# Performance work log

Measured on AMD Instinct MI355X. Metric: run time of the kernel, lower is better.

## Reference

```python
import jax, jax.numpy as jnp
import numpy as np

SCALE = 64 ** -0.5
MAX_LR = 0.01


def newtonschulz5(t, steps=5, eps=1e-7, coefs=(3.4445, -4.775, 2.0315)):
    # t: [h, i, j]; orthogonalize via quintic Newton-Schulz iteration
    a, b, c = coefs
    should_transpose = t.shape[-2] > t.shape[-1]
    if should_transpose:
        t = jnp.swapaxes(t, -1, -2)
    norm = jnp.sqrt(jnp.sum(t * t, axis=(-1, -2), keepdims=True))
    t = t / jnp.maximum(norm, eps)
    for _ in range(steps):
        A = t @ jnp.swapaxes(t, -1, -2)
        B = b * A + c * (A @ A)
        t = a * t + B @ t
    if should_transpose:
        t = jnp.swapaxes(t, -1, -2)
    return t


def setup_inputs() -> dict:
    key = jax.random.key(0)
    ks = jax.random.split(key, 7)
    b, n, d, h, dh = 2, 2048, 512, 8, 64
    s = 0.05  # scale random weights for numerical sanity (softmax not one-hot)
    return {
        "tokens": jax.random.normal(ks[0], (b, n, d), jnp.float32),
        "rms_weight": jnp.ones((d,), jnp.float32),
        "wq": jax.random.normal(ks[1], (h, d, dh), jnp.float32) * s,
        "wk": jax.random.normal(ks[2], (h, d, dh), jnp.float32) * s,
        "wv": jax.random.normal(ks[3], (h, d, dh), jnp.float32) * s,
        "wo": jax.random.normal(ks[4], (h, dh, d), jnp.float32) * s,
        "lr_w": jax.random.normal(ks[5], (1, d), jnp.float32) * s,
        "tv_w": jax.random.normal(ks[6], (d, d), jnp.float32) * s,
        "return_next_memories": 1,
    }


def reference(tokens, rms_weight, wq, wk, wv, wo, lr_w, tv_w, return_next_memories):
    eps = jnp.finfo(tokens.dtype).eps
    # RMSNorm (torch nn.RMSNorm with eps=None -> finfo eps)
    t = tokens * jax.lax.rsqrt(jnp.mean(tokens * tokens, axis=-1, keepdims=True) + eps) * rms_weight

    q = jnp.einsum('bnd,hde->bhne', t, wq)  # [b,h,n,dh]
    k = jnp.einsum('bnd,hde->bhne', t, wk)
    v = jnp.einsum('bnd,hde->bhne', t, wv)

    score = jnp.einsum('bhie,bhje->bhij', q, k) * SCALE
    n = score.shape[-1]
    causal_mask = jnp.triu(jnp.ones((n, n), bool), 1)
    score = jnp.where(causal_mask, -jnp.finfo(score.dtype).max, score)
    attn = jax.nn.softmax(score, axis=-1)
    out = jnp.einsum('bhij,bhje->bhie', attn, v)  # [b,h,n,dh]
    pred_values = jnp.einsum('bhne,hed->bnd', out, wo)

    if not return_next_memories:
        return pred_values

    # target values: Linear(dim,dim,no bias) + LayerNorm(no affine) on shifted tokens
    tv = jnp.einsum('bnd,od->bno', t[:, 1:], tv_w)
    mu = jnp.mean(tv, axis=-1, keepdims=True)
    var = jnp.var(tv, axis=-1, keepdims=True)
    target_values = (tv - mu) * jax.lax.rsqrt(var + 1e-5)

    tok = t[:, :-1]                       # [b,n-1,d]
    pred_fw = pred_values[:, :-1]
    out_t = out[:, :, :-1]
    attn_t = attn[:, :, :-1, :-1]
    q_t, k_t, v_t = q[:, :, :-1], k[:, :, :-1], v[:, :, :-1]

    lr = jax.nn.sigmoid(jnp.einsum('bnd,od->bno', tok, lr_w)) * MAX_LR  # [b,n-1,1]
    error = (target_values - pred_fw) * lr

    dout = jnp.einsum('bnd,hed->bhne', error, wo)            # [b,h,n-1,dh]
    dwo = jnp.einsum('bnd,bhne->hed', error, out_t)          # [h,dh,d]
    delta = jnp.sum(dout * out_t, axis=-1, keepdims=True)    # [b,h,n-1,1]
    dv = jnp.einsum('bhij,bhie->bhje', attn_t, dout)
    dattn = jnp.einsum('bhje,bhie->bhij', v_t, dout)
    dscore = SCALE * attn_t * (dattn - delta)
    dq = jnp.einsum('bhje,bhij->bhie', k_t, dscore)
    dk = jnp.einsum('bhie,bhij->bhje', q_t, dscore)
    dwq = jnp.einsum('bhie,bid->hde', dq, tok)
    dwk = jnp.einsum('bhje,bjd->hde', dk, tok)
    dwv = jnp.einsum('bhje,bjd->hde', dv, tok)

    # muon update: Newton-Schulz orthogonalization of value/output fast-weight grads
    dwv = newtonschulz5(dwv)
    dwo = newtonschulz5(dwo)

    return (pred_values, dwq, dwk, dwv, dwo)
```

## Files before the change

kernel.cpp:

```cpp
#include <hip/hip_runtime.h>
#include <float.h>
#include <math.h>

#define B_   2
#define N_   2048
#define D_   512
#define H_   8
#define DH_  64
#define NM_  2047
#define SCALE_F 0.125f
#define LBK 72

typedef __attribute__((ext_vector_type(8))) short bf16x8;
typedef __attribute__((ext_vector_type(4))) float f32x4;
#define MFMA_B16(a,b,c) __builtin_amdgcn_mfma_f32_16x16x32_bf16(a,b,c,0,0,0)

__device__ __forceinline__ short f2bf(float f){
  unsigned u = __float_as_uint(f);
  unsigned r = u + 0x7fffu + ((u>>16)&1u);
  return (short)(r>>16);
}
__device__ __forceinline__ float bf2f(short s){
  return __uint_as_float(((unsigned)(unsigned short)s)<<16);
}
// ... 121 lines not shown
    outt[(size_t)(c0+rr)*4096 + r0+cc]=l[rr][cc];
  }
}
__global__ __launch_bounds__(256) void k_trans_f(const float* __restrict__ in,
    short* __restrict__ outn, short* __restrict__ outt){
  __shared__ short l[64][66];
  int r0=blockIdx.x<<6, c0=blockIdx.y<<6, tid=threadIdx.x;
  for(int kk=0;kk<16;kk++){
    int idx=kk*256+tid, rr=idx>>6, cc=idx&63;
    short v=f2bf(in[(size_t)(r0+rr)*512 + c0+cc]);
    outn[(size_t)(r0+rr)*512 + c0+cc]=v;
    l[cc][rr]=v;
  }
  __syncthreads();
  for(int kk=0;kk<16;kk++){
    int idx=kk*256+tid, rr=idx>>6, cc=idx&63;
    outt[(size_t)(c0+rr)*4096 + r0+cc]=l[rr][cc];
  }
}

__global__ __launch_bounds__(256) void k_gemm_qkv(const short* __restrict__ tb,
    const short* __restrict__ wqt, const short* __restrict__ wkt, const short* __restrict__ wvt,
    short* __restrict__ qh, short* __restrict__ kh, short* __restrict__ vh,
    short* __restrict__ qt, short* __restrict__ kt, short* __restrict__ vt){
  __shared__ __attribute__((aligned(16))) short as[64][LBK], bs[64][LBK];
  int r0=blockIdx.x<<6, ct=blockIdx.y, which=ct>>3, h=ct&7;
  const short* Bt=(which==0?wqt:which==1?wkt:wvt)+(size_t)h*32768;
  f32x4 acc[4];
  #pragma unroll
  for(int nb=0;nb<4;nb++) acc[nb]=(f32x4){0.f,0.f,0.f,0.f};
  gemm64(tb+(size_t)r0*512, 512, Bt, 512, 8, as, bs, acc);
  short* on=(which==0?qh:which==1?kh:vh);
  short* ot=(which==0?qt:which==1?kt:vt);
  int tid=threadIdx.x, w=tid>>6, lane=tid&63, lg=lane>>4, ln=lane&15;
  size_t bh=(size_t)(r0>>11)*8+h;
  int n0=(r0&2047)+w*16+lg*4;
  #pragma unroll
  for(int nb=0;nb<4;nb++){
    int e=nb*16+ln;
    short4 s4;
    s4.x=f2bf(acc[nb][0]); s4.y=f2bf(acc[nb][1]);
    s4.z=f2bf(acc[nb][2]); s4.w=f2bf(acc[nb][3]);
    on[(bh*2048+n0  )*64+e]=s4.x;
    on[(bh*2048+n0+1)*64+e]=s4.y;
    on[(bh*2048+n0+2)*64+e]=s4.z;
    on[(bh*2048+n0+3)*64+e]=s4.w;
    *(short4*)&ot[(bh*64+e)*2048+n0]=s4;
  }
}

__global__ __launch_bounds__(256) void k_fa_fwd(const short* __restrict__ qh,
    const short* __restrict__ kh, const short* __restrict__ vt,
    float* __restrict__ op0, float* __restrict__ op1, float* __restrict__ mlb){
  int bh = blockIdx.x, qq = blockIdx.y, half = blockIdx.z;
  int it = (qq<16)? (31-qq) : (qq-16);
  int i0 = it<<6;
  const short* qhb = qh + (size_t)bh*N_*DH_;
  const short* khb = kh + (size_t)bh*N_*DH_;
  const short* vtb = vt + (size_t)bh*DH_*N_;
  __shared__ __attribute__((aligned(16))) short ks[64][LBK], vts[64][LBK];
  __shared__ __attribute__((aligned(16))) short psb[4][16][LBK];
  int tid=threadIdx.x, w=tid>>6, lane=tid&63, lg=lane>>4, ln=lane&15;
  bf16x8 aq[2];
  #pragma unroll
  for(int s=0;s<2;s++)
    aq[s] = *(const bf16x8*)&qhb[(size_t)(i0+w*16+ln)*DH_ + 32*s + lg*8];
  f32x4 acc[4];
  float mrow[4], lrow[4];
  #pragma unroll
  for(int nb=0;nb<4;nb++) acc[nb]=(f32x4){0.f,0.f,0.f,0.f};
  #pragma unroll
  for(int r=0;r<4;r++){ mrow[r]=-FLT_MAX; lrow[r]=0.f; }
  int4 ka0,ka1,va0,va1;
  tload(khb+(size_t)half*64*DH_, DH_, tid, ka0,ka1);
  tload(vtb+half*64, N_, tid, va0,va1);
  for(int jt=half;jt<=it;jt+=2){
    int j0 = jt<<6;
    bool diag = (jt==it);
    __syncthreads();
    twrite(ks, tid, ka0,ka1);
    twrite(vts, tid, va0,va1);
    if(jt+2<=it){
      tload(khb+(size_t)(jt+2)*64*DH_, DH_, tid, ka0,ka1);
      tload(vtb+(jt+2)*64, N_, tid, va0,va1);
    }
    __syncthreads();
    f32x4 sv[4];
    __builtin_amdgcn_s_setprio(1);
    #pragma unroll
    for(int nb=0;nb<4;nb++){
      f32x4 z = {0.f,0.f,0.f,0.f};
      #pragma unroll
      for(int s=0;s<2;s++){
        bf16x8 bk = *(const bf16x8*)&ks[nb*16+ln][32*s + lg*8];
        z = MFMA_B16(aq[s], bk, z);
      }
      sv[nb]=z;
    }
    __builtin_amdgcn_s_setprio(0);
    int iiB = i0 + w*16 + lg*4;
    #pragma unroll
    for(int r=0;r<4;r++){
      int ii = iiB + r;
      float srow[4]; float mx = -FLT_MAX;
      if(diag){
        #pragma unroll
        for(int nb=0;nb<4;nb++){
          float x = sv[nb][r]*SCALE_F;
          if(j0+nb*16+ln > ii) x = -FLT_MAX;
          srow[nb]=x; mx=fmaxf(mx,x);
        }
      } else {
        #pragma unroll
        for(int nb=0;nb<4;nb++){
          float x = sv[nb][r]*SCALE_F;
          srow[nb]=x; mx=fmaxf(mx,x);
        }
      }
      mx=fmaxf(mx,__shfl_xor(mx,1)); mx=fmaxf(mx,__shfl_xor(mx,2));
      mx=fmaxf(mx,__shfl_xor(mx,4)); mx=fmaxf(mx,__shfl_xor(mx,8));
      float mn = fmaxf(mrow[r], mx);
      float rs = 0.f;
      #pragma unroll
      for(int nb=0;nb<4;nb++){
        float pv = __expf(srow[nb]-mn);
        psb[w][lg*4+r][ln+16*nb]=f2bf(pv); rs+=pv;
      }
      rs+=__shfl_xor(rs,1); rs+=__shfl_xor(rs,2);
      rs+=__shfl_xor(rs,4); rs+=__shfl_xor(rs,8);
      float corr = __expf(mrow[r]-mn);
      lrow[r]=lrow[r]*corr+rs; mrow[r]=mn;
      #pragma unroll
      for(int nb=0;nb<4;nb++) acc[nb][r]*=corr;
    }
    lds_fence();
    __builtin_amdgcn_s_setprio(1);
    #pragma unroll
    for(int nb=0;nb<4;nb++){
      #pragma unroll
      for(int s=0;s<2;s++){
        bf16x8 pa = *(const bf16x8*)&psb[w][ln][32*s + lg*8];
        bf16x8 bv = *(const bf16x8*)&vts[nb*16+ln][32*s + lg*8];
        acc[nb] = MFMA_B16(pa, bv, acc[nb]);
      }
    }
    __builtin_amdgcn_s_setprio(0);
    lds_fence();
  }
  float* op   = half? op1 : op0;
  float* marr = mlb + half*65536;
  float* larr = marr + 32768;
  #pragma unroll
  for(int r=0;r<4;r++){
    int ii = i0 + w*16 + lg*4 + r;
    size_t row = (size_t)bh*2048 + ii;
    #pragma unroll
    for(int nb=0;nb<4;nb++)
      op[row*64 + nb*16+ln] = acc[nb][r];
    if(ln==0){ marr[row]=mrow[r]; larr[row]=lrow[r]; }
  }
}

__global__ __launch_bounds__(256) void k_fa_merge(const float* __restrict__ op0,
    const float* __restrict__ op1, const float* __restrict__ mlb,
    short* __restrict__ obb, float* __restrict__ lse){
  int row = blockIdx.x*4 + (threadIdx.x>>6);
  int lane = threadIdx.x&63;
  float m0 = mlb[row],        l0 = mlb[32768+row];
  float m1 = mlb[65536+row],  l1 = mlb[98304+row];
  float m  = fmaxf(m0,m1);
  float c0 = __expf(m0-m), c1 = __expf(m1-m);
  float l  = l0*c0 + l1*c1;
  float o  = (op0[(size_t)row*64+lane]*c0 + op1[(size_t)row*64+lane]*c1)/l;
  int bh = row>>11, i = row&2047, b = bh>>3, h = bh&7;
  obb[((size_t)(b*2048+i))*512 + h*64 + lane] = f2bf(o);
  if(lane==0) lse[row] = m + logf(l);
}

__global__ __launch_bounds__(256) void k_gemm_pred(const short* __restrict__ obb,
    const short* __restrict__ wot, float* __restrict__ pred){
  __shared__ __attribute__((aligned(16))) short as[64][LBK], bs[64][LBK];
  int r0=blockIdx.x<<6, c0=blockIdx.y<<6;
  f32x4 acc[4];
  #pragma unroll
  for(int nb=0;nb<4;nb++) acc[nb]=(f32x4){0.f,0.f,0.f,0.f};
  gemm64(obb+(size_t)r0*512, 512, wot+(size_t)c0*512, 512, 8, as, bs, acc);
  int tid=threadIdx.x, w=tid>>6, lane=tid&63, lg=lane>>4, ln=lane&15;
  int row=r0+w*16+lg*4;
  #pragma unroll
  for(int nb=0;nb<4;nb++)
    #pragma unroll
    for(int r=0;r<4;r++)
      pred[(size_t)(row+r)*512 + c0+nb*16+ln]=acc[nb][r];
}

__global__ __launch_bounds__(256) void k_gemm_tv(const short* __restrict__ tb,
    const short* __restrict__ tvwb, float* __restrict__ er){
  __shared__ __attribute__((aligned(16))) short as[64][LBK], bs[64][LBK];
  int r0=blockIdx.x<<6, c0=blockIdx.y<<6;
  f32x4 acc[4];
  #pragma unroll
  for(int nb=0;nb<4;nb++) acc[nb]=(f32x4){0.f,0.f,0.f,0.f};
  gemm64(tb+(size_t)(r0+1)*512, 512, tvwb+(size_t)c0*512, 512, 8, as, bs, acc);
  int tid=threadIdx.x, w=tid>>6, lane=tid&63, lg=lane>>4, ln=lane&15;
  int row=r0+w*16+lg*4;
  #pragma unroll
  for(int nb=0;nb<4;nb++)
    #pragma unroll
    for(int r=0;r<4;r++){
      float v=(((row+r)&2047)==2047)?0.f:acc[nb][r];
      er[(size_t)(row+r)*512 + c0+nb*16+ln]=v;
    }
// ... 20 lines not shown
  float S2=r2[0]+r2[1]+r2[2]+r2[3];
  float S3=r3[0]+r3[1]+r3[2]+r3[3];
  float mu  = S1*(1.f/512.f);
  float var = S2*(1.f/512.f) - mu*mu;
  float rstd= rsqrtf(var + 1e-5f);
  float lr  = 0.01f/(1.f+__expf(-S3));
  tv[tid]     = ((v0-mu)*rstd - pr[tid])*lr;
  tv[tid+256] = ((v1-mu)*rstd - pr[tid+256])*lr;
}

__global__ __launch_bounds__(256) void k_gemm_dout(const short* __restrict__ erb,
    const short* __restrict__ wob, short* __restrict__ doh, short* __restrict__ dot){
  __shared__ __attribute__((aligned(16))) short as[64][LBK], bs[64][LBK];
  int r0=blockIdx.x<<6, h=blockIdx.y;
  f32x4 acc[4];
  #pragma unroll
  for(int nb=0;nb<4;nb++) acc[nb]=(f32x4){0.f,0.f,0.f,0.f};
  gemm64(erb+(size_t)r0*512, 512, wob+(size_t)h*32768, 512, 8, as, bs, acc);
  int tid=threadIdx.x, w=tid>>6, lane=tid&63, lg=lane>>4, ln=lane&15;
  size_t bh=(size_t)(r0>>11)*8+h;
  int n0=(r0&2047)+w*16+lg*4;
  #pragma unroll
  for(int nb=0;nb<4;nb++){
    int e=nb*16+ln;
    short4 s4;
    s4.x=f2bf(acc[nb][0]); s4.y=f2bf(acc[nb][1]);
    s4.z=f2bf(acc[nb][2]); s4.w=f2bf(acc[nb][3]);
    doh[(bh*2048+n0  )*64+e]=s4.x;
    doh[(bh*2048+n0+1)*64+e]=s4.y;
    doh[(bh*2048+n0+2)*64+e]=s4.z;
    doh[(bh*2048+n0+3)*64+e]=s4.w;
    *(short4*)&dot[(bh*64+e)*2048+n0]=s4;
  }
}

__global__ __launch_bounds__(256) void k_delta(const short* __restrict__ doh,
    const short* __restrict__ obb, float* __restrict__ delta){
  int rid = blockIdx.x*4 + (threadIdx.x>>6);
  int lane = threadIdx.x&63;
  if(rid >= B_*H_*NM_) return;
  int b = rid/(H_*NM_); int rem = rid - b*H_*NM_;
  int h = rem/NM_; int i = rem - h*NM_;
  float v = bf2f(doh[((size_t)(b*H_+h)*N_ + i)*DH_ + lane])
          * bf2f(obb[((size_t)(b*N_+i))*D_ + h*DH_ + lane]);
  v = wred64(v);
  if(lane==0) delta[((size_t)(b*H_+h))*N_ + i] = v;
}

__global__ __launch_bounds__(256) void k_fa_dq(const short* __restrict__ qh,
    const short* __restrict__ kh, const short* __restrict__ vh,
    const short* __restrict__ kt, const short* __restrict__ doh,
    const float* __restrict__ lse, const float* __restrict__ delta,
    short* __restrict__ dqt, short* __restrict__ dqp1){
  int bh = blockIdx.x, it = blockIdx.y, half = blockIdx.z;
  int i0 = it<<6;
  const short* qhb = qh + (size_t)bh*N_*DH_;
  const short* khb = kh + (size_t)bh*N_*DH_;
  const short* vhb = vh + (size_t)bh*N_*DH_;
  const short* ktb = kt + (size_t)bh*DH_*N_;
  const short* dohb= doh+ (size_t)bh*N_*DH_;
  __shared__ __attribute__((aligned(16))) short ks[64][LBK], vs[64][LBK], kts[64][LBK];
  __shared__ __attribute__((aligned(16))) short psb[4][16][LBK];
  int tid=threadIdx.x, w=tid>>6, lane=tid&63, lg=lane>>4, ln=lane&15;
  bf16x8 aq[2], ad[2];
  float Lr[4], dl[4];
  #pragma unroll
  for(int s=0;s<2;s++){
    aq[s]=*(const bf16x8*)&qhb[(size_t)(i0+w*16+ln)*DH_+32*s+lg*8];
    ad[s]=*(const bf16x8*)&dohb[(size_t)(i0+w*16+ln)*DH_+32*s+lg*8];
  }
  #pragma unroll
  for(int r=0;r<4;r++){
    int ii=i0+w*16+lg*4+r;
    Lr[r]=lse[(size_t)bh*N_+ii];
    dl[r]=(ii<NM_)?delta[(size_t)bh*N_+ii]:0.f;
  }
  f32x4 acc[4];
  #pragma unroll
  for(int nb=0;nb<4;nb++) acc[nb]=(f32x4){0.f,0.f,0.f,0.f};
  int4 ka0,ka1,va0,va1,ta0,ta1;
  tload(khb+(size_t)half*64*DH_, DH_, tid, ka0,ka1);
  tload(vhb+(size_t)half*64*DH_, DH_, tid, va0,va1);
  tload(ktb+half*64, N_, tid, ta0,ta1);
  for(int jt=half;jt<=it;jt+=2){
    int j0=jt<<6;
    bool msk_needed = (jt==it) || (it==31);
    __syncthreads();
    twrite(ks, tid, ka0,ka1);
    twrite(vs, tid, va0,va1);
    twrite(kts, tid, ta0,ta1);
    if(jt+2<=it){
      tload(khb+(size_t)(jt+2)*64*DH_, DH_, tid, ka0,ka1);
      tload(vhb+(size_t)(jt+2)*64*DH_, DH_, tid, va0,va1);
      tload(ktb+(jt+2)*64, N_, tid, ta0,ta1);
    }
    __syncthreads();
    f32x4 sv[4], dav[4];
    __builtin_amdgcn_s_setprio(1);
    #pragma unroll
    for(int nb=0;nb<4;nb++){
      f32x4 z={0.f,0.f,0.f,0.f}, zd={0.f,0.f,0.f,0.f};
      #pragma unroll
      for(int s=0;s<2;s++){
        bf16x8 bk=*(const bf16x8*)&ks[nb*16+ln][32*s+lg*8];
        bf16x8 bv=*(const bf16x8*)&vs[nb*16+ln][32*s+lg*8];
        z = MFMA_B16(aq[s], bk, z);
        zd= MFMA_B16(ad[s], bv, zd);
      }
      sv[nb]=z; dav[nb]=zd;
    }
    __builtin_amdgcn_s_setprio(0);
    if(msk_needed){
      #pragma unroll
      for(int r=0;r<4;r++){
        int ii=i0+w*16+lg*4+r;
        #pragma unroll
        for(int nb=0;nb<4;nb++){
          int jj=j0+nb*16+ln;
          float pv=__expf(sv[nb][r]*SCALE_F - Lr[r]);
          float dsv=SCALE_F*pv*(dav[nb][r]-dl[r]);
          if(jj>ii || ii>=NM_ || jj>=NM_) dsv=0.f;
          psb[w][lg*4+r][ln+16*nb]=f2bf(dsv);
        }
      }
    } else {
      #pragma unroll
      for(int r=0;r<4;r++)
        #pragma unroll
        for(int nb=0;nb<4;nb++){
          float pv=__expf(sv[nb][r]*SCALE_F - Lr[r]);
          psb[w][lg*4+r][ln+16*nb]=f2bf(SCALE_F*pv*(dav[nb][r]-dl[r]));
        }
    }
    lds_fence();
    __builtin_amdgcn_s_setprio(1);
    #pragma unroll
    for(int nb=0;nb<4;nb++){
      #pragma unroll
      for(int s=0;s<2;s++){
        bf16x8 pa = *(const bf16x8*)&psb[w][ln][32*s+lg*8];
        bf16x8 bk = *(const bf16x8*)&kts[nb*16+ln][32*s+lg*8];
        acc[nb]=MFMA_B16(pa,bk,acc[nb]);
      }
    }
    __builtin_amdgcn_s_setprio(0);
    lds_fence();
  }
  short* dst = half? dqp1 : dqt;
  #pragma unroll
  for(int nb=0;nb<4;nb++){
    short4 s4;
    s4.x=f2bf(acc[nb][0]); s4.y=f2bf(acc[nb][1]);
    s4.z=f2bf(acc[nb][2]); s4.w=f2bf(acc[nb][3]);
    *(short4*)&dst[((size_t)bh*64 + nb*16+ln)*2048 + i0+w*16+lg*4]=s4;
  }
}

__global__ __launch_bounds__(256) void k_dqred(short* __restrict__ dqt,
    const short* __restrict__ dqp1){
  size_t i = ((size_t)blockIdx.x*256 + threadIdx.x)*8;
  int4 a = *(const int4*)&dqt[i];
  int4 b = *(const int4*)&dqp1[i];
  short* pa=(short*)&a; const short* pb=(const short*)&b;
  short out[8];
  #pragma unroll
  for(int k=0;k<8;k++) out[k]=f2bf(bf2f(pa[k])+bf2f(pb[k]));
  *(int4*)&dqt[i] = *(int4*)out;
}

__global__ __launch_bounds__(256) void k_fa_dkv(const short* __restrict__ kh,
    const short* __restrict__ vh, const short* __restrict__ qh,
    const short* __restrict__ qt, const short* __restrict__ doh,
    const short* __restrict__ dot,
    const float* __restrict__ lse, const float* __restrict__ delta,
    short* __restrict__ dkt, short* __restrict__ dvt,
    short* __restrict__ dkp1, short* __restrict__ dvp1){
  int bh = blockIdx.x, jt = blockIdx.y, half = blockIdx.z;
  int j0 = jt<<6;
  const short* khb = kh + (size_t)bh*N_*DH_;
  const short* vhb = vh + (size_t)bh*N_*DH_;
  const short* qhb = qh + (size_t)bh*N_*DH_;
  const short* qtb = qt + (size_t)bh*DH_*N_;
  const short* dohb= doh+ (size_t)bh*N_*DH_;
  const short* dotb= dot+ (size_t)bh*DH_*N_;
  __shared__ __attribute__((aligned(16))) short qs[64][LBK], dos[64][LBK], qts[64][LBK], dots[64][LBK];
  __shared__ __attribute__((aligned(16))) short psv[4][16][LBK], psk[4][16][LBK];
  __shared__ float Ls[64], dls[64];
  int tid=threadIdx.x, w=tid>>6, lane=tid&63, lg=lane>>4, ln=lane&15;
  bf16x8 akf[2], avf[2];
  #pragma unroll
  for(int s=0;s<2;s++){
    akf[s]=*(const bf16x8*)&khb[(size_t)(j0+w*16+ln)*DH_+32*s+lg*8];
    avf[s]=*(const bf16x8*)&vhb[(size_t)(j0+w*16+ln)*DH_+32*s+lg*8];
  }
  f32x4 accv[4], acck[4];
  #pragma unroll
  for(int nb=0;nb<4;nb++){
    accv[nb]=(f32x4){0.f,0.f,0.f,0.f};
    acck[nb]=(f32x4){0.f,0.f,0.f,0.f};
  }
  int it0 = jt + half;
  int4 qa0,qa1,da0,da1,qta0,qta1,dta0,dta1;
  float Lnx=0.f, dlnx=0.f;
  {
    int ip = (it0<32)? (it0<<6) : 0;
    tload(qhb+(size_t)ip*DH_, DH_, tid, qa0,qa1);
    tload(dohb+(size_t)ip*DH_, DH_, tid, da0,da1);
    tload(qtb+ip, N_, tid, qta0,qta1);
    tload(dotb+ip, N_, tid, dta0,dta1);
    if(tid<64){
      int ii=ip+tid;
      Lnx=lse[(size_t)bh*N_+ii];
      dlnx=(ii<NM_)?delta[(size_t)bh*N_+ii]:0.f;
    }
  }
  for(int it=it0; it<32; it+=2){
    int i0=it<<6;
    bool msk_needed = (it==jt) || (it==31);
    __syncthreads();
    twrite(qs, tid, qa0,qa1);
    twrite(dos, tid, da0,da1);
    twrite(qts, tid, qta0,qta1);
    twrite(dots, tid, dta0,dta1);
    if(tid<64){ Ls[tid]=Lnx; dls[tid]=dlnx; }
    if(it+2<32){
      int i1=(it+2)<<6;
      tload(qhb+(size_t)i1*DH_, DH_, tid, qa0,qa1);
      tload(dohb+(size_t)i1*DH_, DH_, tid, da0,da1);
      tload(qtb+i1, N_, tid, qta0,qta1);
      tload(dotb+i1, N_, tid, dta0,dta1);
      if(tid<64){
        int ii=i1+tid;
        Lnx=lse[(size_t)bh*N_+ii];
        dlnx=(ii<NM_)?delta[(size_t)bh*N_+ii]:0.f;
      }
    }
    __syncthreads();
    f32x4 sv[4], dav[4];
    __builtin_amdgcn_s_setprio(1);
    #pragma unroll
    for(int nb=0;nb<4;nb++){
      f32x4 z={0.f,0.f,0.f,0.f}, zd={0.f,0.f,0.f,0.f};
      #pragma unroll
      for(int s=0;s<2;s++){
        bf16x8 bq=*(const bf16x8*)&qs[nb*16+ln][32*s+lg*8];
        bf16x8 bd=*(const bf16x8*)&dos[nb*16+ln][32*s+lg*8];
        z = MFMA_B16(akf[s], bq, z);
        zd= MFMA_B16(avf[s], bd, zd);
      }
      sv[nb]=z; dav[nb]=zd;
    }
    __builtin_amdgcn_s_setprio(0);
    if(msk_needed){
      #pragma unroll
      for(int nb=0;nb<4;nb++){
        float Lc=Ls[nb*16+ln], dlc=dls[nb*16+ln];
        int ii=i0+nb*16+ln;
        #pragma unroll
        for(int r=0;r<4;r++){
          int jj=j0+w*16+lg*4+r;
          float pv=__expf(sv[nb][r]*SCALE_F - Lc);
          bool msk=(jj>ii)||(ii>=NM_)||(jj>=NM_);
          if(msk) pv=0.f;
          float ds = msk?0.f: SCALE_F*pv*(dav[nb][r]-dlc);
          psv[w][lg*4+r][ln+16*nb]=f2bf(pv);
          psk[w][lg*4+r][ln+16*nb]=f2bf(ds);
        }
      }
    } else {
      #pragma unroll
      for(int nb=0;nb<4;nb++){
        float Lc=Ls[nb*16+ln], dlc=dls[nb*16+ln];
        #pragma unroll
        for(int r=0;r<4;r++){
          float pv=__expf(sv[nb][r]*SCALE_F - Lc);
          psv[w][lg*4+r][ln+16*nb]=f2bf(pv);
          psk[w][lg*4+r][ln+16*nb]=f2bf(SCALE_F*pv*(dav[nb][r]-dlc));
        }
      }
    }
    lds_fence();
    __builtin_amdgcn_s_setprio(1);
    #pragma unroll
    for(int nb=0;nb<4;nb++){
      #pragma unroll
      for(int s=0;s<2;s++){
        bf16x8 pa = *(const bf16x8*)&psv[w][ln][32*s+lg*8];
        bf16x8 bd = *(const bf16x8*)&dots[nb*16+ln][32*s+lg*8];
        accv[nb]=MFMA_B16(pa,bd,accv[nb]);
        bf16x8 pk = *(const bf16x8*)&psk[w][ln][32*s+lg*8];
        bf16x8 bq = *(const bf16x8*)&qts[nb*16+ln][32*s+lg*8];
        acck[nb]=MFMA_B16(pk,bq,acck[nb]);
      }
    }
    __builtin_amdgcn_s_setprio(0);
    lds_fence();
  }
  short* dvd = half? dvp1 : dvt;
  short* dkd = half? dkp1 : dkt;
  #pragma unroll
  for(int nb=0;nb<4;nb++){
    int e=nb*16+ln, n0=j0+w*16+lg*4;
    short4 s4;
    s4.x=f2bf(accv[nb][0]); s4.y=f2bf(accv[nb][1]);
    s4.z=f2bf(accv[nb][2]); s4.w=f2bf(accv[nb][3]);
    *(short4*)&dvd[((size_t)bh*64+e)*2048 + n0]=s4;
    s4.x=f2bf(acck[nb][0]); s4.y=f2bf(acck[nb][1]);
    s4.z=f2bf(acck[nb][2]); s4.w=f2bf(acck[nb][3]);
    *(short4*)&dkd[((size_t)bh*64+e)*2048 + n0]=s4;
  }
}

__global__ __launch_bounds__(256) void k_dkvred(short* __restrict__ dkt,
    short* __restrict__ dvt, const short* __restrict__ dkp1,
    const short* __restrict__ dvp1){
  int bid = blockIdx.x;
  short* dst; const short* src;
  if(bid<1024){ dst=dkt; src=dkp1; } else { dst=dvt; src=dvp1; bid-=1024; }
  size_t i = ((size_t)bid*256 + threadIdx.x)*8;
  int4 a = *(const int4*)&dst[i];
  int4 b = *(const int4*)&src[i];
  short* pa=(short*)&a; const short* pb=(const short*)&b;
  short out[8];
  #pragma unroll
  for(int k=0;k<8;k++) out[k]=f2bf(bf2f(pa[k])+bf2f(pb[k]));
  *(int4*)&dst[i] = *(int4*)out;
}

__global__ __launch_bounds__(256) void k_gemm_wgq(const short* __restrict__ tt,
    const short* __restrict__ g, float* __restrict__ par){
  __shared__ __attribute__((aligned(16))) short as[64][LBK], bs[64][LBK];
  int dt=blockIdx.x, h=blockIdx.y, sp=blockIdx.z;
  int b=sp>>2, n0b=(sp&3)*512;
  f32x4 acc[4];
  #pragma unroll
  for(int nb=0;nb<4;nb++) acc[nb]=(f32x4){0.f,0.f,0.f,0.f};
  gemm64(tt + (size_t)(dt*64)*4096 + sp*512, 4096,
         g  + ((size_t)(b*8+h)*64)*2048 + n0b, 2048, 8, as, bs, acc);
  int tid=threadIdx.x, w=tid>>6, lane=tid&63, lg=lane>>4, ln=lane&15;
  int row=w*16+lg*4;
  #pragma unroll
  for(int nb=0;nb<4;nb++)
    #pragma unroll
    for(int r=0;r<4;r++)
      par[(size_t)sp*262144 + (size_t)h*32768 + (size_t)(dt*64+row+r)*64 + nb*16+ln]=acc[nb][r];
}

__global__ __launch_bounds__(256) void k_gemm_wgo(const short* __restrict__ outt,
    const short* __restrict__ ert, float* __restrict__ par){
  __shared__ __attribute__((aligned(16))) short as[64][LBK], bs[64][LBK];
  int ct=blockIdx.x, h=blockIdx.y, sp=blockIdx.z;
  f32x4 acc[4];
  #pragma unroll
  for(int nb=0;nb<4;nb++) acc[nb]=(f32x4){0.f,0.f,0.f,0.f};
  gemm64(outt + (size_t)(h*64)*4096 + sp*512, 4096,
         ert  + (size_t)(ct*64)*4096 + sp*512, 4096, 8, as, bs, acc);
  int tid=threadIdx.x, w=tid>>6, lane=tid&63, lg=lane>>4, ln=lane&15;
  int row=w*16+lg*4;
  #pragma unroll
  for(int nb=0;nb<4;nb++)
    #pragma unroll
    for(int r=0;r<4;r++)
// ... 125 lines not shown
  const float* wq   =(const float*)d_in[2];
  const float* wk   =(const float*)d_in[3];
  const float* wv   =(const float*)d_in[4];
  const float* wo   =(const float*)d_in[5];
  const float* lrw  =(const float*)d_in[6];
  const float* tvw  =(const float*)d_in[7];
  float* out = (float*)d_out;
  float* ws  = (float*)d_ws;

  short* tb   = (short*)(ws);
  short* tt   = (short*)(ws + 1064960);
  short* qh   = (short*)(ws + 2113536);
  short* kh   = (short*)(ws + 3162112);
  short* vh   = (short*)(ws + 4210688);
  short* qt   = (short*)(ws + 5259264);
  short* kt   = (short*)(ws + 6307840);
  short* vt   = (short*)(ws + 7356416);
  float* er_  = ws + 8404992;
  float* op0  = ws + 8404992;
  short* dqp1 = (short*)(ws + 8404992);
  short* dkp1 = (short*)(ws + 8404992);
  short* dvp1 = (short*)(ws + 9453568);
  short* obb  = (short*)(ws + 10502144);
  short* outt = (short*)(ws + 11550720);
  short* erb  = (short*)(ws + 12599296);
  short* ert  = (short*)(ws + 13647872);
  short* doh  = (short*)(ws + 14696448);
  short* dot  = (short*)(ws + 15745024);
  float* par_ = ws + 14696448;
  float* op1  = ws + 14696448;
  short* dqt  = (short*)(ws + 16793600);
  float* mlb  = ws + 16793600;
  short* dkt  = (short*)(ws + 17842176);
  short* dvt  = (short*)(ws + 18890752);
  short* wqt  = (short*)(ws + 19939328);
  short* wkt  = (short*)(ws + 20070400);
  short* wvt  = (short*)(ws + 20201472);
  short* wob  = (short*)(ws + 20332544);
  short* wot  = (short*)(ws + 20463616);
  short* tvwb = (short*)(ws + 20594688);
  float* lse_ = ws + 20725760;
  float* dlt_ = ws + 20758528;
  float* X0_  = ws + 20791296;

  float* OUT_PRED = out;
  float* OUT_DWQ  = out + 2097152;
  float* OUT_DWK  = out + 2359296;
  float* OUT_DWV  = out + 2621440;
  float* OUT_DWO  = out + 2883584;

  k_rmsnorm<<<4160,256,0,stream>>>(tokens, rmsw, tb);
  k_wprep<<<272,256,0,stream>>>(wq,wk,wv,wo,tvw, wqt,wkt,wvt,wob,wot,tvwb);
  k_gemm_qkv<<<dim3(64,24),256,0,stream>>>(tb, wqt,wkt,wvt, qh,kh,vh, qt,kt,vt);
  k_fa_fwd<<<dim3(16,32,2),256,0,stream>>>(qh, kh, vt, op0, op1, mlb);
  k_fa_merge<<<8192,256,0,stream>>>(op0, op1, mlb, obb, lse_);
  k_gemm_pred<<<dim3(64,8),256,0,stream>>>(obb, wot, OUT_PRED);

  if(out_size < 3145728) return;

  k_trans_b<<<dim3(64,8),256,0,stream>>>(tb, tt);
  k_gemm_tv<<<dim3(64,8),256,0,stream>>>(tb, tvwb, er_);
  k_lnerr<<<4094,256,0,stream>>>(er_, tb, OUT_PRED, lrw);
  k_trans_f<<<dim3(64,8),256,0,stream>>>(er_, erb, ert);
  k_gemm_dout<<<dim3(64,8),256,0,stream>>>(erb, wob, doh, dot);
  k_delta<<<8188,256,0,stream>>>(doh, obb, dlt_);
  k_fa_dq<<<dim3(16,32,2),256,0,stream>>>(qh, kh, vh, kt, doh, lse_, dlt_, dqt, dqp1);
  k_dqred<<<1024,256,0,stream>>>(dqt, dqp1);
  k_fa_dkv<<<dim3(16,32,2),256,0,stream>>>(kh, vh, qh, qt, doh, dot, lse_, dlt_,
                                           dkt, dvt, dkp1, dvp1);
  k_dkvred<<<2048,256,0,stream>>>(dkt, dvt, dkp1, dvp1);
  k_trans_b<<<dim3(64,8),256,0,stream>>>(obb, outt);

  k_gemm_wgq<<<dim3(8,8,8),256,0,stream>>>(tt, dqt, par_);
  k_wred_direct<<<1024,256,0,stream>>>(par_, OUT_DWQ);
  k_gemm_wgq<<<dim3(8,8,8),256,0,stream>>>(tt, dkt, par_);
  k_wred_direct<<<1024,256,0,stream>>>(par_, OUT_DWK);
  k_gemm_wgq<<<dim3(8,8,8),256,0,stream>>>(tt, dvt, par_);
  k_wred_xv<<<1024,256,0,stream>>>(par_, X0_);
  k_gemm_wgo<<<dim3(8,8,8),256,0,stream>>>(outt, ert, par_);
  k_wred_xo<<<1024,256,0,stream>>>(par_, X0_);

  k_ns_fused<<<16,1024,0,stream>>>(X0_, OUT_DWV, OUT_DWO);
}
```

Baseline: 311.1 us.

## Process two adjacent 64-row tiles per block in flash-attention kernels

The forward, dQ and dKV attention kernels now have each block handle a pair of adjacent query (or key) tiles. Every K/V (or Q/dO) tile staged into LDS is reused for both tiles, and the grid is halved from 1024 to 512 blocks. Blocks are paired so work stays balanced across the causal triangle. This cuts global-to-LDS traffic and barrier count per unit of work, at the cost of roughly double the registers and LDS per block and fewer blocks to spread across the CUs.

```diff
diff --git a/kernel.cpp b/kernel.cpp
--- a/kernel.cpp
+++ b/kernel.cpp
@@ -197,86 +197,102 @@
 __global__ __launch_bounds__(256) void k_fa_fwd(const short* __restrict__ qh,
     const short* __restrict__ kh, const short* __restrict__ vt,
     float* __restrict__ op0, float* __restrict__ op1, float* __restrict__ mlb){
-  int bh = blockIdx.x, qq = blockIdx.y, half = blockIdx.z;
-  int it = (qq<16)? (31-qq) : (qq-16);
-  int i0 = it<<6;
+  int bh = blockIdx.x, y = blockIdx.y;
+  int a    = (y<16)? y : 31-y;
+  int half = (y<16)? 0 : 1;
+  int itA = 2*a, itB = 2*a+1;
   const short* qhb = qh + (size_t)bh*N_*DH_;
   const short* khb = kh + (size_t)bh*N_*DH_;
   const short* vtb = vt + (size_t)bh*DH_*N_;
   __shared__ __attribute__((aligned(16))) short ks[64][LBK], vts[64][LBK];
-  __shared__ __attribute__((aligned(16))) short psb[4][16][LBK];
+  __shared__ __attribute__((aligned(16))) short psb[2][4][16][LBK];
   int tid=threadIdx.x, w=tid>>6, lane=tid&63, lg=lane>>4, ln=lane&15;
-  bf16x8 aq[2];
-  #pragma unroll
-  for(int s=0;s<2;s++)
-    aq[s] = *(const bf16x8*)&qhb[(size_t)(i0+w*16+ln)*DH_ + 32*s + lg*8];
-  f32x4 acc[4];
-  float mrow[4], lrow[4];
-  #pragma unroll
-  for(int nb=0;nb<4;nb++) acc[nb]=(f32x4){0.f,0.f,0.f,0.f};
-  #pragma unroll
-  for(int r=0;r<4;r++){ mrow[r]=-FLT_MAX; lrow[r]=0.f; }
+  bf16x8 aq[2][2];
+  #pragma unroll
+  for(int sd=0;sd<2;sd++){
+    int i0=(sd?itB:itA)<<6;
+    #pragma unroll
+    for(int s=0;s<2;s++)
+      aq[sd][s] = *(const bf16x8*)&qhb[(size_t)(i0+w*16+ln)*DH_ + 32*s + lg*8];
+  }
+  f32x4 acc[2][4];
+  float mrow[2][4], lrow[2][4];
+  #pragma unroll
+  for(int sd=0;sd<2;sd++){
+    #pragma unroll
+    for(int nb=0;nb<4;nb++) acc[sd][nb]=(f32x4){0.f,0.f,0.f,0.f};
+    #pragma unroll
+    for(int r=0;r<4;r++){ mrow[sd][r]=-FLT_MAX; lrow[sd][r]=0.f; }
+  }
   int4 ka0,ka1,va0,va1;
   tload(khb+(size_t)half*64*DH_, DH_, tid, ka0,ka1);
   tload(vtb+half*64, N_, tid, va0,va1);
-  for(int jt=half;jt<=it;jt+=2){
+  for(int jt=half;jt<=itB;jt+=2){
     int j0 = jt<<6;
-    bool diag = (jt==it);
+    bool actA = (jt<=itA);
     __syncthreads();
     twrite(ks, tid, ka0,ka1);
     twrite(vts, tid, va0,va1);
-    if(jt+2<=it){
+    if(jt+2<=itB){
       tload(khb+(size_t)(jt+2)*64*DH_, DH_, tid, ka0,ka1);
       tload(vtb+(jt+2)*64, N_, tid, va0,va1);
     }
     __syncthreads();
-    f32x4 sv[4];
+    f32x4 sv[2][4];
     __builtin_amdgcn_s_setprio(1);
     #pragma unroll
     for(int nb=0;nb<4;nb++){
-      f32x4 z = {0.f,0.f,0.f,0.f};
+      f32x4 z0={0.f,0.f,0.f,0.f}, z1={0.f,0.f,0.f,0.f};
       #pragma unroll
       for(int s=0;s<2;s++){
         bf16x8 bk = *(const bf16x8*)&ks[nb*16+ln][32*s + lg*8];
-        z = MFMA_B16(aq[s], bk, z);
-      }
-      sv[nb]=z;
+        z0 = MFMA_B16(aq[0][s], bk, z0);
+        z1 = MFMA_B16(aq[1][s], bk, z1);
+      }
+      sv[0][nb]=z0; sv[1][nb]=z1;
     }
     __builtin_amdgcn_s_setprio(0);
-    int iiB = i0 + w*16 + lg*4;
-    #pragma unroll
-    for(int r=0;r<4;r++){
-      int ii = iiB + r;
-      float srow[4]; float mx = -FLT_MAX;
-      if(diag){
+    #pragma unroll
+    for(int sd=0;sd<2;sd++){
+      if(sd==0 && !actA) continue;
+      int it_ = sd? itB : itA;
+      int i0  = it_<<6;
+      bool diag = (jt==it_);
+      int iiB = i0 + w*16 + lg*4;
+      #pragma unroll
+      for(int r=0;r<4;r++){
+        int ii = iiB + r;
+        float srow[4]; float mx = -FLT_MAX;
+        if(diag){
+          #pragma unroll
+          for(int nb=0;nb<4;nb++){
+            float x = sv[sd][nb][r]*SCALE_F;
+            if(j0+nb*16+ln > ii) x = -FLT_MAX;
+            srow[nb]=x; mx=fmaxf(mx,x);
+          }
+        } else {
+          #pragma unroll
+          for(int nb=0;nb<4;nb++){
+            float x = sv[sd][nb][r]*SCALE_F;
+            srow[nb]=x; mx=fmaxf(mx,x);
+          }
+        }
+        mx=fmaxf(mx,__shfl_xor(mx,1)); mx=fmaxf(mx,__shfl_xor(mx,2));
+        mx=fmaxf(mx,__shfl_xor(mx,4)); mx=fmaxf(mx,__shfl_xor(mx,8));
+        float mn = fmaxf(mrow[sd][r], mx);
+        float rs = 0.f;
         #pragma unroll
         for(int nb=0;nb<4;nb++){
-          float x = sv[nb][r]*SCALE_F;
-          if(j0+nb*16+ln > ii) x = -FLT_MAX;
-          srow[nb]=x; mx=fmaxf(mx,x);
+          float pv = __expf(srow[nb]-mn);
+          psb[sd][w][lg*4+r][ln+16*nb]=f2bf(pv); rs+=pv;
         }
-      } else {
+        rs+=__shfl_xor(rs,1); rs+=__shfl_xor(rs,2);
+        rs+=__shfl_xor(rs,4); rs+=__shfl_xor(rs,8);
+        float corr = __expf(mrow[sd][r]-mn);
+        lrow[sd][r]=lrow[sd][r]*corr+rs; mrow[sd][r]=mn;
         #pragma unroll
-        for(int nb=0;nb<4;nb++){
-          float x = sv[nb][r]*SCALE_F;
-          srow[nb]=x; mx=fmaxf(mx,x);
-        }
-      }
-      mx=fmaxf(mx,__shfl_xor(mx,1)); mx=fmaxf(mx,__shfl_xor(mx,2));
-      mx=fmaxf(mx,__shfl_xor(mx,4)); mx=fmaxf(mx,__shfl_xor(mx,8));
-      float mn = fmaxf(mrow[r], mx);
-      float rs = 0.f;
-      #pragma unroll
-      for(int nb=0;nb<4;nb++){
-        float pv = __expf(srow[nb]-mn);
-        psb[w][lg*4+r][ln+16*nb]=f2bf(pv); rs+=pv;
-      }
-      rs+=__shfl_xor(rs,1); rs+=__shfl_xor(rs,2);
-      rs+=__shfl_xor(rs,4); rs+=__shfl_xor(rs,8);
-      float corr = __expf(mrow[r]-mn);
-      lrow[r]=lrow[r]*corr+rs; mrow[r]=mn;
-      #pragma unroll
-      for(int nb=0;nb<4;nb++) acc[nb][r]*=corr;
+        for(int nb=0;nb<4;nb++) acc[sd][nb][r]*=corr;
+      }
     }
     lds_fence();
     __builtin_amdgcn_s_setprio(1);
@@ -284,9 +300,13 @@
     for(int nb=0;nb<4;nb++){
       #pragma unroll
       for(int s=0;s<2;s++){
-        bf16x8 pa = *(const bf16x8*)&psb[w][ln][32*s + lg*8];
         bf16x8 bv = *(const bf16x8*)&vts[nb*16+ln][32*s + lg*8];
-        acc[nb] = MFMA_B16(pa, bv, acc[nb]);
+        bf16x8 pa1 = *(const bf16x8*)&psb[1][w][ln][32*s + lg*8];
+        acc[1][nb] = MFMA_B16(pa1, bv, acc[1][nb]);
+        if(actA){
+          bf16x8 pa0 = *(const bf16x8*)&psb[0][w][ln][32*s + lg*8];
+          acc[0][nb] = MFMA_B16(pa0, bv, acc[0][nb]);
+        }
       }
     }
     __builtin_amdgcn_s_setprio(0);
@@ -296,13 +316,17 @@
   float* marr = mlb + half*65536;
   float* larr = marr + 32768;
   #pragma unroll
-  for(int r=0;r<4;r++){
-    int ii = i0 + w*16 + lg*4 + r;
-    size_t row = (size_t)bh*2048 + ii;
-    #pragma unroll
-    for(int nb=0;nb<4;nb++)
-      op[row*64 + nb*16+ln] = acc[nb][r];
-    if(ln==0){ marr[row]=mrow[r]; larr[row]=lrow[r]; }
+  for(int sd=0;sd<2;sd++){
+    int i0=(sd?itB:itA)<<6;
+    #pragma unroll
+    for(int r=0;r<4;r++){
+      int ii = i0 + w*16 + lg*4 + r;
+      size_t row = (size_t)bh*2048 + ii;
+      #pragma unroll
+      for(int nb=0;nb<4;nb++)
+        op[row*64 + nb*16+ln] = acc[sd][nb][r];
+      if(ln==0){ marr[row]=mrow[sd][r]; larr[row]=lrow[sd][r]; }
+    }
   }
 }
 
@@ -429,85 +453,96 @@
     const short* __restrict__ kt, const short* __restrict__ doh,
     const float* __restrict__ lse, const float* __restrict__ delta,
     short* __restrict__ dqt, short* __restrict__ dqp1){
-  int bh = blockIdx.x, it = blockIdx.y, half = blockIdx.z;
-  int i0 = it<<6;
+  int bh = blockIdx.x, y = blockIdx.y;
+  int a    = (y<16)? y : 31-y;
+  int half = (y<16)? 0 : 1;
+  int itA = 2*a, itB = 2*a+1;
   const short* qhb = qh + (size_t)bh*N_*DH_;
   const short* khb = kh + (size_t)bh*N_*DH_;
   const short* vhb = vh + (size_t)bh*N_*DH_;
   const short* ktb = kt + (size_t)bh*DH_*N_;
   const short* dohb= doh+ (size_t)bh*N_*DH_;
   __shared__ __attribute__((aligned(16))) short ks[64][LBK], vs[64][LBK], kts[64][LBK];
-  __shared__ __attribute__((aligned(16))) short psb[4][16][LBK];
+  __shared__ __attribute__((aligned(16))) short psb[2][4][16][LBK];
   int tid=threadIdx.x, w=tid>>6, lane=tid&63, lg=lane>>4, ln=lane&15;
-  bf16x8 aq[2], ad[2];
-  float Lr[4], dl[4];
-  #pragma unroll
-  for(int s=0;s<2;s++){
-    aq[s]=*(const bf16x8*)&qhb[(size_t)(i0+w*16+ln)*DH_+32*s+lg*8];
-    ad[s]=*(const bf16x8*)&dohb[(size_t)(i0+w*16+ln)*DH_+32*s+lg*8];
-  }
-  #pragma unroll
-  for(int r=0;r<4;r++){
-    int ii=i0+w*16+lg*4+r;
-    Lr[r]=lse[(size_t)bh*N_+ii];
-    dl[r]=(ii<NM_)?delta[(size_t)bh*N_+ii]:0.f;
-  }
-  f32x4 acc[4];
-  #pragma unroll
-  for(int nb=0;nb<4;nb++) acc[nb]=(f32x4){0.f,0.f,0.f,0.f};
+  bf16x8 aq[2][2], ad[2][2];
+  float Lr[2][4], dl[2][4];
+  #pragma unroll
+  for(int sd=0;sd<2;sd++){
+    int i0=(sd?itB:itA)<<6;
+    #pragma unroll
+    for(int s=0;s<2;s++){
+      aq[sd][s]=*(const bf16x8*)&qhb[(size_t)(i0+w*16+ln)*DH_+32*s+lg*8];
+      ad[sd][s]=*(const bf16x8*)&dohb[(size_t)(i0+w*16+ln)*DH_+32*s+lg*8];
+    }
+    #pragma unroll
+    for(int r=0;r<4;r++){
+      int ii=i0+w*16+lg*4+r;
+      Lr[sd][r]=lse[(size_t)bh*N_+ii];
+      dl[sd][r]=(ii<NM_)?delta[(size_t)bh*N_+ii]:0.f;
+    }
+  }
+  f32x4 acc[2][4];
+  #pragma unroll
+  for(int sd=0;sd<2;sd++)
+    #pragma unroll
+    for(int nb=0;nb<4;nb++) acc[sd][nb]=(f32x4){0.f,0.f,0.f,0.f};
   int4 ka0,ka1,va0,va1,ta0,ta1;
   tload(khb+(size_t)half*64*DH_, DH_, tid, ka0,ka1);
   tload(vhb+(size_t)half*64*DH_, DH_, tid, va0,va1);
   tload(ktb+half*64, N_, tid, ta0,ta1);
-  for(int jt=half;jt<=it;jt+=2){
+  for(int jt=half;jt<=itB;jt+=2){
     int j0=jt<<6;
-    bool msk_needed = (jt==it) || (it==31);
+    bool actA = (jt<=itA);
     __syncthreads();
     twrite(ks, tid, ka0,ka1);
     twrite(vs, tid, va0,va1);
     twrite(kts, tid, ta0,ta1);
-    if(jt+2<=it){
+    if(jt+2<=itB){
       tload(khb+(size_t)(jt+2)*64*DH_, DH_, tid, ka0,ka1);
       tload(vhb+(size_t)(jt+2)*64*DH_, DH_, tid, va0,va1);
       tload(ktb+(jt+2)*64, N_, tid, ta0,ta1);
     }
     __syncthreads();
-    f32x4 sv[4], dav[4];
-    __builtin_amdgcn_s_setprio(1);
     #pragma unroll
     for(int nb=0;nb<4;nb++){
-      f32x4 z={0.f,0.f,0.f,0.f}, zd={0.f,0.f,0.f,0.f};
+      f32x4 z0={0.f,0.f,0.f,0.f}, zd0={0.f,0.f,0.f,0.f};
+      f32x4 z1={0.f,0.f,0.f,0.f}, zd1={0.f,0.f,0.f,0.f};
+      __builtin_amdgcn_s_setprio(1);
       #pragma unroll
       for(int s=0;s<2;s++){
         bf16x8 bk=*(const bf16x8*)&ks[nb*16+ln][32*s+lg*8];
         bf16x8 bv=*(const bf16x8*)&vs[nb*16+ln][32*s+lg*8];
-        z = MFMA_B16(aq[s], bk, z);
-        zd= MFMA_B16(ad[s], bv, zd);
-      }
-      sv[nb]=z; dav[nb]=zd;
-    }
-    __builtin_amdgcn_s_setprio(0);
-    if(msk_needed){
-      #pragma unroll
-      for(int r=0;r<4;r++){
-        int ii=i0+w*16+lg*4+r;
-        #pragma unroll
-        for(int nb=0;nb<4;nb++){
-          int jj=j0+nb*16+ln;
-          float pv=__expf(sv[nb][r]*SCALE_F - Lr[r]);
-          float dsv=SCALE_F*pv*(dav[nb][r]-dl[r]);
-          if(jj>ii || ii>=NM_ || jj>=NM_) dsv=0.f;
-          psb[w][lg*4+r][ln+16*nb]=f2bf(dsv);
+        z0 = MFMA_B16(aq[0][s], bk, z0);
+        zd0= MFMA_B16(ad[0][s], bv, zd0);
+        z1 = MFMA_B16(aq[1][s], bk, z1);
+        zd1= MFMA_B16(ad[1][s], bv, zd1);
+      }
+      __builtin_amdgcn_s_setprio(0);
+      #pragma unroll
+      for(int sd=0;sd<2;sd++){
+        if(sd==0 && !actA) continue;
+        int it_ = sd? itB : itA;
+        f32x4 z  = sd? z1 : z0;
+        f32x4 zd = sd? zd1: zd0;
+        if((jt==it_)||(it_==31)){
+          int i0=it_<<6;
+          #pragma unroll
+          for(int r=0;r<4;r++){
+            int ii=i0+w*16+lg*4+r, jj=j0+nb*16+ln;
+            float pv=__expf(z[r]*SCALE_F - Lr[sd][r]);
+            float dsv=SCALE_F*pv*(zd[r]-dl[sd][r]);
+            if(jj>ii || ii>=NM_ || jj>=NM_) dsv=0.f;
+            psb[sd][w][lg*4+r][ln+16*nb]=f2bf(dsv);
+          }
+        } else {
+          #pragma unroll
+          for(int r=0;r<4;r++){
+            float pv=__expf(z[r]*SCALE_F - Lr[sd][r]);
+            psb[sd][w][lg*4+r][ln+16*nb]=f2bf(SCALE_F*pv*(zd[r]-dl[sd][r]));
+          }
         }
       }
-    } else {
-      #pragma unroll
-      for(int r=0;r<4;r++)
-        #pragma unroll
-        for(int nb=0;nb<4;nb++){
-          float pv=__expf(sv[nb][r]*SCALE_F - Lr[r]);
-          psb[w][lg*4+r][ln+16*nb]=f2bf(SCALE_F*pv*(dav[nb][r]-dl[r]));
-        }
     }
     lds_fence();
     __builtin_amdgcn_s_setprio(1);
@@ -515,9 +550,13 @@
     for(int nb=0;nb<4;nb++){
       #pragma unroll
       for(int s=0;s<2;s++){
-        bf16x8 pa = *(const bf16x8*)&psb[w][ln][32*s+lg*8];
-        bf16x8 bk = *(const bf16x8*)&kts[nb*16+ln][32*s+lg*8];
-        acc[nb]=MFMA_B16(pa,bk,acc[nb]);
+        bf16x8 bkt = *(const bf16x8*)&kts[nb*16+ln][32*s+lg*8];
+        bf16x8 pa1 = *(const bf16x8*)&psb[1][w][ln][32*s+lg*8];
+        acc[1][nb]=MFMA_B16(pa1,bkt,acc[1][nb]);
+        if(actA){
+          bf16x8 pa0 = *(const bf16x8*)&psb[0][w][ln][32*s+lg*8];
+          acc[0][nb]=MFMA_B16(pa0,bkt,acc[0][nb]);
+        }
       }
     }
     __builtin_amdgcn_s_setprio(0);
@@ -525,11 +564,15 @@
   }
   short* dst = half? dqp1 : dqt;
   #pragma unroll
-  for(int nb=0;nb<4;nb++){
-    short4 s4;
-    s4.x=f2bf(acc[nb][0]); s4.y=f2bf(acc[nb][1]);
-    s4.z=f2bf(acc[nb][2]); s4.w=f2bf(acc[nb][3]);
-    *(short4*)&dst[((size_t)bh*64 + nb*16+ln)*2048 + i0+w*16+lg*4]=s4;
+  for(int sd=0;sd<2;sd++){
+    int i0=(sd?itB:itA)<<6;
+    #pragma unroll
+    for(int nb=0;nb<4;nb++){
+      short4 s4;
+      s4.x=f2bf(acc[sd][nb][0]); s4.y=f2bf(acc[sd][nb][1]);
+      s4.z=f2bf(acc[sd][nb][2]); s4.w=f2bf(acc[sd][nb][3]);
+      *(short4*)&dst[((size_t)bh*64 + nb*16+ln)*2048 + i0+w*16+lg*4]=s4;
+    }
   }
 }
 
@@ -552,8 +595,11 @@
     const float* __restrict__ lse, const float* __restrict__ delta,
     short* __restrict__ dkt, short* __restrict__ dvt,
     short* __restrict__ dkp1, short* __restrict__ dvp1){
-  int bh = blockIdx.x, jt = blockIdx.y, half = blockIdx.z;
-  int j0 = jt<<6;
+  int bh = blockIdx.x, y = blockIdx.y;
+  int a    = (y<16)? y : 31-y;
+  int half = (y<16)? 0 : 1;
+  int jtA = 2*a, jtB = 2*a+1;
+  int j0A = jtA<<6, j0B = jtB<<6;
   const short* khb = kh + (size_t)bh*N_*DH_;
   const short* vhb = vh + (size_t)bh*N_*DH_;
   const short* qhb = qh + (size_t)bh*N_*DH_;
@@ -561,26 +607,32 @@
   const short* dohb= doh+ (size_t)bh*N_*DH_;
   const short* dotb= dot+ (size_t)bh*DH_*N_;
   __shared__ __attribute__((aligned(16))) short qs[64][LBK], dos[64][LBK], qts[64][LBK], dots[64][LBK];
-  __shared__ __attribute__((aligned(16))) short psv[4][16][LBK], psk[4][16][LBK];
+  __shared__ __attribute__((aligned(16))) short psv[2][4][16][LBK], psk[2][4][16][LBK];
   __shared__ float Ls[64], dls[64];
   int tid=threadIdx.x, w=tid>>6, lane=tid&63, lg=lane>>4, ln=lane&15;
-  bf16x8 akf[2], avf[2];
-  #pragma unroll
-  for(int s=0;s<2;s++){
-    akf[s]=*(const bf16x8*)&khb[(size_t)(j0+w*16+ln)*DH_+32*s+lg*8];
-    avf[s]=*(const bf16x8*)&vhb[(size_t)(j0+w*16+ln)*DH_+32*s+lg*8];
-  }
-  f32x4 accv[4], acck[4];
-  #pragma unroll
-  for(int nb=0;nb<4;nb++){
-    accv[nb]=(f32x4){0.f,0.f,0.f,0.f};
-    acck[nb]=(f32x4){0.f,0.f,0.f,0.f};
-  }
-  int it0 = jt + half;
+  bf16x8 akf[2][2], avf[2][2];
+  #pragma unroll
+  for(int sd=0;sd<2;sd++){
+    int j0=(sd?jtB:jtA)<<6;
+    #pragma unroll
+    for(int s=0;s<2;s++){
+      akf[sd][s]=*(const bf16x8*)&khb[(size_t)(j0+w*16+ln)*DH_+32*s+lg*8];
+      avf[sd][s]=*(const bf16x8*)&vhb[(size_t)(j0+w*16+ln)*DH_+32*s+lg*8];
+    }
+  }
+  f32x4 accv[2][4], acck[2][4];
+  #pragma unroll
+  for(int sd=0;sd<2;sd++)
+    #pragma unroll
+    for(int nb=0;nb<4;nb++){
+      accv[sd][nb]=(f32x4){0.f,0.f,0.f,0.f};
+      acck[sd][nb]=(f32x4){0.f,0.f,0.f,0.f};
+    }
+  int it0 = jtA + half;
   int4 qa0,qa1,da0,da1,qta0,qta1,dta0,dta1;
   float Lnx=0.f, dlnx=0.f;
   {
-    int ip = (it0<32)? (it0<<6) : 0;
+    int ip = it0<<6;
     tload(qhb+(size_t)ip*DH_, DH_, tid, qa0,qa1);
     tload(dohb+(size_t)ip*DH_, DH_, tid, da0,da1);
     tload(qtb+ip, N_, tid, qta0,qta1);
@@ -593,7 +645,7 @@
   }
   for(int it=it0; it<32; it+=2){
     int i0=it<<6;
-    bool msk_needed = (it==jt) || (it==31);
+    bool actB = (it>=jtB);
     __syncthreads();
     twrite(qs, tid, qa0,qa1);
     twrite(dos, tid, da0,da1);
@@ -613,46 +665,48 @@
       }
     }
     __syncthreads();
-    f32x4 sv[4], dav[4];
-    __builtin_amdgcn_s_setprio(1);
     #pragma unroll
     for(int nb=0;nb<4;nb++){
-      f32x4 z={0.f,0.f,0.f,0.f}, zd={0.f,0.f,0.f,0.f};
+      f32x4 z0={0.f,0.f,0.f,0.f}, zd0={0.f,0.f,0.f,0.f};
+      f32x4 z1={0.f,0.f,0.f,0.f}, zd1={0.f,0.f,0.f,0.f};
+      __builtin_amdgcn_s_setprio(1);
       #pragma unroll
       for(int s=0;s<2;s++){
         bf16x8 bq=*(const bf16x8*)&qs[nb*16+ln][32*s+lg*8];
         bf16x8 bd=*(const bf16x8*)&dos[nb*16+ln][32*s+lg*8];
-        z = MFMA_B16(akf[s], bq, z);
-        zd= MFMA_B16(avf[s], bd, zd);
-      }
-      sv[nb]=z; dav[nb]=zd;
-    }
-    __builtin_amdgcn_s_setprio(0);
-    if(msk_needed){
-      #pragma unroll
-      for(int nb=0;nb<4;nb++){
-        float Lc=Ls[nb*16+ln], dlc=dls[nb*16+ln];
-        int ii=i0+nb*16+ln;
-        #pragma unroll
-        for(int r=0;r<4;r++){
-          int jj=j0+w*16+lg*4+r;
-          float pv=__expf(sv[nb][r]*SCALE_F - Lc);
-          bool msk=(jj>ii)||(ii>=NM_)||(jj>=NM_);
-          if(msk) pv=0.f;
-          float ds = msk?0.f: SCALE_F*pv*(dav[nb][r]-dlc);
-          psv[w][lg*4+r][ln+16*nb]=f2bf(pv);
-          psk[w][lg*4+r][ln+16*nb]=f2bf(ds);
-        }
-      }
-    } else {
-      #pragma unroll
-      for(int nb=0;nb<4;nb++){
-        float Lc=Ls[nb*16+ln], dlc=dls[nb*16+ln];
-        #pragma unroll
-        for(int r=0;r<4;r++){
-          float pv=__expf(sv[nb][r]*SCALE_F - Lc);
-          psv[w][lg*4+r][ln+16*nb]=f2bf(pv);
-          psk[w][lg*4+r][ln+16*nb]=f2bf(SCALE_F*pv*(dav[nb][r]-dlc));
+        z0 = MFMA_B16(akf[0][s], bq, z0);
+        zd0= MFMA_B16(avf[0][s], bd, zd0);
+        z1 = MFMA_B16(akf[1][s], bq, z1);
+        zd1= MFMA_B16(avf[1][s], bd, zd1);
+      }
+      __builtin_amdgcn_s_setprio(0);
+      float Lc=Ls[nb*16+ln], dlc=dls[nb*16+ln];
+      int ii=i0+nb*16+ln;
+      #pragma unroll
+      for(int sd=0;sd<2;sd++){
+        if(sd==1 && !actB) continue;
+        int jt_ = sd? jtB : jtA;
+        int j0_ = sd? j0B : j0A;
+        f32x4 z  = sd? z1 : z0;
+        f32x4 zd = sd? zd1: zd0;
+        if((it==jt_)||(it==31)){
+          #pragma unroll
+          for(int r=0;r<4;r++){
+            int jj=j0_+w*16+lg*4+r;
+            float pv=__expf(z[r]*SCALE_F - Lc);
+            bool msk=(jj>ii)||(ii>=NM_)||(jj>=NM_);
+            if(msk) pv=0.f;
+            float ds = msk?0.f: SCALE_F*pv*(zd[r]-dlc);
+            psv[sd][w][lg*4+r][ln+16*nb]=f2bf(pv);
+            psk[sd][w][lg*4+r][ln+16*nb]=f2bf(ds);
+          }
+        } else {
+          #pragma unroll
+          for(int r=0;r<4;r++){
+            float pv=__expf(z[r]*SCALE_F - Lc);
+            psv[sd][w][lg*4+r][ln+16*nb]=f2bf(pv);
+            psk[sd][w][lg*4+r][ln+16*nb]=f2bf(SCALE_F*pv*(zd[r]-dlc));
+          }
         }
       }
     }
@@ -662,12 +716,18 @@
     for(int nb=0;nb<4;nb++){
       #pragma unroll
       for(int s=0;s<2;s++){
-        bf16x8 pa = *(const bf16x8*)&psv[w][ln][32*s+lg*8];
         bf16x8 bd = *(const bf16x8*)&dots[nb*16+ln][32*s+lg*8];
-        accv[nb]=MFMA_B16(pa,bd,accv[nb]);
-        bf16x8 pk = *(const bf16x8*)&psk[w][ln][32*s+lg*8];
         bf16x8 bq = *(const bf16x8*)&qts[nb*16+ln][32*s+lg*8];
-        acck[nb]=MFMA_B16(pk,bq,acck[nb]);
+        bf16x8 pa0 = *(const bf16x8*)&psv[0][w][ln][32*s+lg*8];
+        accv[0][nb]=MFMA_B16(pa0,bd,accv[0][nb]);
+        bf16x8 pk0 = *(const bf16x8*)&psk[0][w][ln][32*s+lg*8];
+        acck[0][nb]=MFMA_B16(pk0,bq,acck[0][nb]);
+        if(actB){
+          bf16x8 pa1 = *(const bf16x8*)&psv[1][w][ln][32*s+lg*8];
+          accv[1][nb]=MFMA_B16(pa1,bd,accv[1][nb]);
+          bf16x8 pk1 = *(const bf16x8*)&psk[1][w][ln][32*s+lg*8];
+          acck[1][nb]=MFMA_B16(pk1,bq,acck[1][nb]);
+        }
       }
     }
     __builtin_amdgcn_s_setprio(0);
@@ -676,15 +736,19 @@
   short* dvd = half? dvp1 : dvt;
   short* dkd = half? dkp1 : dkt;
   #pragma unroll
-  for(int nb=0;nb<4;nb++){
-    int e=nb*16+ln, n0=j0+w*16+lg*4;
-    short4 s4;
-    s4.x=f2bf(accv[nb][0]); s4.y=f2bf(accv[nb][1]);
-    s4.z=f2bf(accv[nb][2]); s4.w=f2bf(accv[nb][3]);
-    *(short4*)&dvd[((size_t)bh*64+e)*2048 + n0]=s4;
-    s4.x=f2bf(acck[nb][0]); s4.y=f2bf(acck[nb][1]);
-    s4.z=f2bf(acck[nb][2]); s4.w=f2bf(acck[nb][3]);
-    *(short4*)&dkd[((size_t)bh*64+e)*2048 + n0]=s4;
+  for(int sd=0;sd<2;sd++){
+    int j0=(sd?jtB:jtA)<<6;
+    #pragma unroll
+    for(int nb=0;nb<4;nb++){
+      int e=nb*16+ln, n0=j0+w*16+lg*4;
+      short4 s4;
+      s4.x=f2bf(accv[sd][nb][0]); s4.y=f2bf(accv[sd][nb][1]);
+      s4.z=f2bf(accv[sd][nb][2]); s4.w=f2bf(accv[sd][nb][3]);
+      *(short4*)&dvd[((size_t)bh*64+e)*2048 + n0]=s4;
+      s4.x=f2bf(acck[sd][nb][0]); s4.y=f2bf(acck[sd][nb][1]);
+      s4.z=f2bf(acck[sd][nb][2]); s4.w=f2bf(acck[sd][nb][3]);
+      *(short4*)&dkd[((size_t)bh*64+e)*2048 + n0]=s4;
+    }
   }
 }
 
@@ -916,7 +980,7 @@
   k_rmsnorm<<<4160,256,0,stream>>>(tokens, rmsw, tb);
   k_wprep<<<272,256,0,stream>>>(wq,wk,wv,wo,tvw, wqt,wkt,wvt,wob,wot,tvwb);
   k_gemm_qkv<<<dim3(64,24),256,0,stream>>>(tb, wqt,wkt,wvt, qh,kh,vh, qt,kt,vt);
-  k_fa_fwd<<<dim3(16,32,2),256,0,stream>>>(qh, kh, vt, op0, op1, mlb);
+  k_fa_fwd<<<dim3(16,32),256,0,stream>>>(qh, kh, vt, op0, op1, mlb);
   k_fa_merge<<<8192,256,0,stream>>>(op0, op1, mlb, obb, lse_);
   k_gemm_pred<<<dim3(64,8),256,0,stream>>>(obb, wot, OUT_PRED);
 
@@ -928,10 +992,10 @@
   k_trans_f<<<dim3(64,8),256,0,stream>>>(er_, erb, ert);
   k_gemm_dout<<<dim3(64,8),256,0,stream>>>(erb, wob, doh, dot);
   k_delta<<<8188,256,0,stream>>>(doh, obb, dlt_);
-  k_fa_dq<<<dim3(16,32,2),256,0,stream>>>(qh, kh, vh, kt, doh, lse_, dlt_, dqt, dqp1);
+  k_fa_dq<<<dim3(16,32),256,0,stream>>>(qh, kh, vh, kt, doh, lse_, dlt_, dqt, dqp1);
   k_dqred<<<1024,256,0,stream>>>(dqt, dqp1);
-  k_fa_dkv<<<dim3(16,32,2),256,0,stream>>>(kh, vh, qh, qt, doh, dot, lse_, dlt_,
-                                           dkt, dvt, dkp1, dvp1);
+  k_fa_dkv<<<dim3(16,32),256,0,stream>>>(kh, vh, qh, qt, doh, dot, lse_, dlt_,
+                                         dkt, dvt, dkp1, dvp1);
   k_dkvred<<<2048,256,0,stream>>>(dkt, dvt, dkp1, dvp1);
   k_trans_b<<<dim3(64,8),256,0,stream>>>(obb, outt);
 
```

Result: slower. 352.9 us (+13.4%).
